# Performance work log

Measured on AMD Instinct MI355X. Metric: run time of the kernel, lower is better.

The kernel has to match this reference:

```python
import jax, jax.numpy as jnp
import numpy as np

DT = 0.02          # full control timestep (cfg dt)
N_SUBSTEPS = 8     # RK4 substeps per forward call
LMBDA = 0.5        # first-order actuator lag gain
G_VEC = jnp.array([0.0, 0.0, -9.81], dtype=jnp.float32)
N_ENVS = 2097152


def setup_inputs() -> dict:
    key = jax.random.key(0)
    k1, k2 = jax.random.split(key)
    X0 = jax.random.normal(k1, (N_ENVS, 9), dtype=jnp.float32)
    U = jax.random.normal(k2, (N_ENVS, 3), dtype=jnp.float32)
    return {"X0": X0, "U": U}


def reference(X0, U):
    h = DT / N_SUBSTEPS  # substep size

    def dynamics(X):
        v = X[:, 3:6]
        a = X[:, 6:9]
        a_dot = LMBDA * (U - a) / DT   # actuator lag uses full dt, as in torch code
        # X_dot = [p_dot, v_dot, a_dot] = [v, a - g_vec, a_dot]
        return jnp.concatenate([v, a - G_VEC, a_dot], axis=-1)

    def rk4_step(X, _):
        k1 = dynamics(X)
        k2 = dynamics(X + 0.5 * h * k1)
        k3 = dynamics(X + 0.5 * h * k2)
        k4 = dynamics(X + h * k3)
        X_next = X + (h / 6.0) * (k1 + 2.0 * k2 + 2.0 * k3 + k4)
        return X_next, None

    X_final, _ = jax.lax.scan(rk4_step, X0, None, length=N_SUBSTEPS)
    return X_final
```

## Files before the change

kernel.cpp:

```cpp
#include <hip/hip_runtime.h>


#define THREADS 256
#define TILE 256
#define CHUNK 4

struct Coeffs {
    float P00, P01, P02;
    float P10, P11, P12;
    float P20, P21, P22;
    float Ku0, Ku1, Ku2;
    float Kg0, Kg1, Kg2;
};

__device__ __forceinline__ void barrier_lgkm() {
    asm volatile("s_waitcnt lgkmcnt(0)" ::: "memory");
    __builtin_amdgcn_s_barrier();
    asm volatile("" ::: "memory");
}

__device__ __forceinline__ void compute_env(const float* __restrict__ sx,
                                            const float* __restrict__ su,
                                            const Coeffs& cf, float r[9]) {
    #pragma unroll
    for (int k = 0; k < 3; ++k) {
        const float p = sx[k];
        const float v = sx[3 + k];
        const float a = sx[6 + k];
        const float u = su[k];
        const float g = (k == 2) ? -9.81f : 0.0f;
        r[k]     = cf.P00 * p + cf.P01 * v + cf.P02 * a + cf.Ku0 * u + cf.Kg0 * g;
        r[3 + k] = cf.P10 * p + cf.P11 * v + cf.P12 * a + cf.Ku1 * u + cf.Kg1 * g;
        r[6 + k] = cf.P20 * p + cf.P21 * v + cf.P22 * a + cf.Ku2 * u + cf.Kg2 * g;
    }
}

__global__ __launch_bounds__(THREADS)
void pointmass_kernel(const float* __restrict__ X0,
                      const float* __restrict__ U,
                      float* __restrict__ Out,
                      int envTotal, Coeffs cf) {
    __shared__ float s_x[2][TILE * 9];
    __shared__ float s_u[2][TILE * 3];

    const int t = threadIdx.x;
    const int tileTotal = (envTotal + TILE - 1) / TILE;
    const int tb = blockIdx.x * CHUNK;
    if (tb >= tileTotal) return;
    const int te = min(tb + CHUNK, tileTotal);

    const bool allFull = (te * TILE <= envTotal);

    if (allFull) {
        const float4* X4 = (const float4*)X0;
        const float4* U4 = (const float4*)U;
        float4* O4 = (float4*)Out;

        {
            const size_t xb = (size_t)tb * 576;
            const size_t ub = (size_t)tb * 192;
            float4 a0 = X4[xb + t];
            float4 a1 = X4[xb + t + 256];
            float4 a2 = make_float4(0.f, 0.f, 0.f, 0.f);
            float4 b0 = make_float4(0.f, 0.f, 0.f, 0.f);
            if (t < 64)  a2 = X4[xb + t + 512];
            if (t < 192) b0 = U4[ub + t];
            ((float4*)s_x[0])[t]       = a0;
            ((float4*)s_x[0])[t + 256] = a1;
            if (t < 64)  ((float4*)s_x[0])[t + 512] = a2;
            if (t < 192) ((float4*)s_u[0])[t]       = b0;
        }
        barrier_lgkm();

        int cur = 0;
        for (int i = tb; i < te; ++i) {
            const bool haveNext = (i + 1 < te);

            float4 a0, a1;
            float4 a2 = make_float4(0.f, 0.f, 0.f, 0.f);
            float4 b0 = make_float4(0.f, 0.f, 0.f, 0.f);
            if (haveNext) {
                const size_t xb = (size_t)(i + 1) * 576;
                const size_t ub = (size_t)(i + 1) * 192;
                a0 = X4[xb + t];
                a1 = X4[xb + t + 256];
                if (t < 64)  a2 = X4[xb + t + 512];
                if (t < 192) b0 = U4[ub + t];
            }

            {
                float r[9];
                compute_env(s_x[cur] + t * 9, s_u[cur] + t * 3, cf, r);
                float* sxw = s_x[cur] + t * 9;
                #pragma unroll
                for (int q = 0; q < 9; ++q) sxw[q] = r[q];
            }
            barrier_lgkm();

            {
                const size_t ob = (size_t)i * 576;
                O4[ob + t]       = ((const float4*)s_x[cur])[t];
                O4[ob + t + 256] = ((const float4*)s_x[cur])[t + 256];
                if (t < 64) O4[ob + t + 512] = ((const float4*)s_x[cur])[t + 512];
            }

            if (haveNext) {
                const int nxt = cur ^ 1;
                ((float4*)s_x[nxt])[t]       = a0;
                ((float4*)s_x[nxt])[t + 256] = a1;
                if (t < 64)  ((float4*)s_x[nxt])[t + 512] = a2;
                if (t < 192) ((float4*)s_u[nxt])[t]       = b0;
                barrier_lgkm();
                cur = nxt;
            }
        }
    } else {
        for (int i = tb; i < te; ++i) {
            const int base = i * TILE;
            const int n = min(TILE, envTotal - base);
            __syncthreads();
            for (int j = t; j < n * 9; j += THREADS)
                s_x[0][j] = X0[(size_t)base * 9 + j];
            for (int j = t; j < n * 3; j += THREADS)
                s_u[0][j] = U[(size_t)base * 3 + j];
            __syncthreads();
            if (t < n) {
                float r[9];
                compute_env(s_x[0] + t * 9, s_u[0] + t * 3, cf, r);
                #pragma unroll
                for (int q = 0; q < 9; ++q)
                    Out[((size_t)base + t) * 9 + q] = r[q];
            }
        }
    }
}

static void mat3_mul(const double A[3][3], const double B[3][3], double C[3][3]) {
    for (int i = 0; i < 3; ++i)
        for (int j = 0; j < 3; ++j) {
            double s = 0.0;
            for (int k = 0; k < 3; ++k) s += A[i][k] * B[k][j];
            C[i][j] = s;
        }
}
static void mat3_copy(const double A[3][3], double B[3][3]) {
    for (int i = 0; i < 3; ++i) for (int j = 0; j < 3; ++j) B[i][j] = A[i][j];
}

extern "C" void kernel_launch(void* const* d_in, const int* in_sizes, int n_in,
                              void* d_out, int out_size, void* d_ws, size_t ws_size,
                              hipStream_t stream) {
    const float* X0 = (const float*)d_in[0];
    const float* U  = (const float*)d_in[1];
    float* Out = (float*)d_out;
    const int envTotal = in_sizes[0] / 9;

    const double DT = 0.02;
    const double h = DT / 8.0;
    const double c = 0.5 / DT;
    double hA[3][3] = {{0, h, 0}, {0, 0, h}, {0, 0, -c * h}};

    double hA2[3][3], hA3[3][3], hA4[3][3];
    mat3_mul(hA, hA, hA2);
    mat3_mul(hA2, hA, hA3);
    mat3_mul(hA3, hA, hA4);

    double P[3][3], Q[3][3];
    for (int i = 0; i < 3; ++i)
        for (int j = 0; j < 3; ++j) {
            const double I = (i == j) ? 1.0 : 0.0;
            P[i][j] = I + hA[i][j] + hA2[i][j] / 2.0 + hA3[i][j] / 6.0 + hA4[i][j] / 24.0;
            Q[i][j] = h * (I + hA[i][j] / 2.0 + hA2[i][j] / 6.0 + hA3[i][j] / 24.0);
        }

    double P2[3][3], P4[3][3], P8[3][3];
    mat3_mul(P, P, P2);
    mat3_mul(P2, P2, P4);
    mat3_mul(P4, P4, P8);

    double IP[3][3], IP2[3][3], IP4[3][3], T[3][3], S[3][3], R[3][3];
    mat3_copy(P, IP);  mat3_copy(P2, IP2);  mat3_copy(P4, IP4);
    for (int i = 0; i < 3; ++i) { IP[i][i] += 1.0; IP2[i][i] += 1.0; IP4[i][i] += 1.0; }
    mat3_mul(IP, IP2, T);
    mat3_mul(T, IP4, S);
    mat3_mul(S, Q, R);

    Coeffs cf;
    cf.P00 = (float)P8[0][0]; cf.P01 = (float)P8[0][1]; cf.P02 = (float)P8[0][2];
    cf.P10 = (float)P8[1][0]; cf.P11 = (float)P8[1][1]; cf.P12 = (float)P8[1][2];
    cf.P20 = (float)P8[2][0]; cf.P21 = (float)P8[2][1]; cf.P22 = (float)P8[2][2];
    cf.Ku0 = (float)(R[0][2] * c); cf.Ku1 = (float)(R[1][2] * c); cf.Ku2 = (float)(R[2][2] * c);
    cf.Kg0 = (float)(-R[0][1]);    cf.Kg1 = (float)(-R[1][1]);    cf.Kg2 = (float)(-R[2][1]);

    const int tileTotal = (envTotal + TILE - 1) / TILE;
    const int blocks = (tileTotal + CHUNK - 1) / CHUNK;
    pointmass_kernel<<<blocks, THREADS, 0, stream>>>(X0, U, Out, envTotal, cf);
}
```

Measured before the change: 157.0 us.

## Make each wavefront own private LDS tiles to drop block-wide barriers

Each 64-lane wavefront now stages and processes its own 64-environment tiles in a private LDS slice, so the block-wide s_barrier calls are removed. Waves then progress independently, and the same double-buffered prefetch is kept per wave. A sched_barrier keeps the compiler from reordering the next-tile LDS writes ahead of the output reads. Trade-offs: the global load and store granularity per wave gets smaller, and the tail is handled by a simple scalar path in the last block.

Result: no change. 156.1 us (-0.5%).

```diff
diff --git a/kernel.cpp b/kernel.cpp
--- a/kernel.cpp
+++ b/kernel.cpp
@@ -2,8 +2,11 @@
 
 
 #define THREADS 256
-#define TILE 256
+#define WAVES 4
+#define WTILE 64
 #define CHUNK 4
+#define XF4 144
+#define UF4 48
 
 struct Coeffs {
     float P00, P01, P02;
@@ -12,12 +15,6 @@
     float Ku0, Ku1, Ku2;
     float Kg0, Kg1, Kg2;
 };
-
-__device__ __forceinline__ void barrier_lgkm() {
-    asm volatile("s_waitcnt lgkmcnt(0)" ::: "memory");
-    __builtin_amdgcn_s_barrier();
-    asm volatile("" ::: "memory");
-}
 
 __device__ __forceinline__ void compute_env(const float* __restrict__ sx,
                                             const float* __restrict__ su,
@@ -40,97 +37,98 @@
                       const float* __restrict__ U,
                       float* __restrict__ Out,
                       int envTotal, Coeffs cf) {
-    __shared__ float s_x[2][TILE * 9];
-    __shared__ float s_u[2][TILE * 3];
+    __shared__ float lds[2][WAVES][768];
 
     const int t = threadIdx.x;
-    const int tileTotal = (envTotal + TILE - 1) / TILE;
-    const int tb = blockIdx.x * CHUNK;
-    if (tb >= tileTotal) return;
-    const int te = min(tb + CHUNK, tileTotal);
+    const int w = t >> 6;
+    const int l = t & 63;
+    const int fullTiles = envTotal / WTILE;
+    const int tileBase = (blockIdx.x * WAVES + w) * CHUNK;
+    const int te = min(tileBase + CHUNK, fullTiles);
 
-    const bool allFull = (te * TILE <= envTotal);
+    const float4* X4 = (const float4*)X0;
+    const float4* U4 = (const float4*)U;
+    float4* O4 = (float4*)Out;
 
-    if (allFull) {
-        const float4* X4 = (const float4*)X0;
-        const float4* U4 = (const float4*)U;
-        float4* O4 = (float4*)Out;
+    if (tileBase < te) {
+        float* const xs0 = &lds[0][w][0];
+        float* const us0 = &lds[0][w][576];
+        float* const xs1 = &lds[1][w][0];
+        float* const us1 = &lds[1][w][576];
 
         {
-            const size_t xb = (size_t)tb * 576;
-            const size_t ub = (size_t)tb * 192;
-            float4 a0 = X4[xb + t];
-            float4 a1 = X4[xb + t + 256];
+            const size_t xb = (size_t)tileBase * XF4;
+            const size_t ub = (size_t)tileBase * UF4;
+            float4 a0 = X4[xb + l];
+            float4 a1 = X4[xb + 64 + l];
             float4 a2 = make_float4(0.f, 0.f, 0.f, 0.f);
             float4 b0 = make_float4(0.f, 0.f, 0.f, 0.f);
-            if (t < 64)  a2 = X4[xb + t + 512];
-            if (t < 192) b0 = U4[ub + t];
-            ((float4*)s_x[0])[t]       = a0;
-            ((float4*)s_x[0])[t + 256] = a1;
-            if (t < 64)  ((float4*)s_x[0])[t + 512] = a2;
-            if (t < 192) ((float4*)s_u[0])[t]       = b0;
+            if (l < 16) a2 = X4[xb + 128 + l];
+            if (l < 48) b0 = U4[ub + l];
+            ((float4*)xs0)[l]      = a0;
+            ((float4*)xs0)[64 + l] = a1;
+            if (l < 16) ((float4*)xs0)[128 + l] = a2;
+            if (l < 48) ((float4*)us0)[l]       = b0;
         }
-        barrier_lgkm();
 
         int cur = 0;
-        for (int i = tb; i < te; ++i) {
+        for (int i = tileBase; i < te; ++i) {
+            float* const xs  = cur ? xs1 : xs0;
+            float* const us  = cur ? us1 : us0;
+            float* const xsN = cur ? xs0 : xs1;
+            float* const usN = cur ? us0 : us1;
             const bool haveNext = (i + 1 < te);
 
             float4 a0, a1;
             float4 a2 = make_float4(0.f, 0.f, 0.f, 0.f);
             float4 b0 = make_float4(0.f, 0.f, 0.f, 0.f);
             if (haveNext) {
-                const size_t xb = (size_t)(i + 1) * 576;
-                const size_t ub = (size_t)(i + 1) * 192;
-                a0 = X4[xb + t];
-                a1 = X4[xb + t + 256];
-                if (t < 64)  a2 = X4[xb + t + 512];
-                if (t < 192) b0 = U4[ub + t];
+                const size_t xb = (size_t)(i + 1) * XF4;
+                const size_t ub = (size_t)(i + 1) * UF4;
+                a0 = X4[xb + l];
+                a1 = X4[xb + 64 + l];
+                if (l < 16) a2 = X4[xb + 128 + l];
+                if (l < 48) b0 = U4[ub + l];
             }
 
             {
                 float r[9];
-                compute_env(s_x[cur] + t * 9, s_u[cur] + t * 3, cf, r);
-                float* sxw = s_x[cur] + t * 9;
+                compute_env(xs + l * 9, us + l * 3, cf, r);
+                float* sxw = xs + l * 9;
                 #pragma unroll
                 for (int q = 0; q < 9; ++q) sxw[q] = r[q];
             }
-            barrier_lgkm();
 
             {
-                const size_t ob = (size_t)i * 576;
-                O4[ob + t]       = ((const float4*)s_x[cur])[t];
-                O4[ob + t + 256] = ((const float4*)s_x[cur])[t + 256];
-                if (t < 64) O4[ob + t + 512] = ((const float4*)s_x[cur])[t + 512];
+                const size_t ob = (size_t)i * XF4;
+                O4[ob + l]      = ((const float4*)xs)[l];
+                O4[ob + 64 + l] = ((const float4*)xs)[64 + l];
+                if (l < 16) O4[ob + 128 + l] = ((const float4*)xs)[128 + l];
             }
 
+            __builtin_amdgcn_sched_barrier(0);
+
             if (haveNext) {
-                const int nxt = cur ^ 1;
-                ((float4*)s_x[nxt])[t]       = a0;
-                ((float4*)s_x[nxt])[t + 256] = a1;
-                if (t < 64)  ((float4*)s_x[nxt])[t + 512] = a2;
-                if (t < 192) ((float4*)s_u[nxt])[t]       = b0;
-                barrier_lgkm();
-                cur = nxt;
+                ((float4*)xsN)[l]      = a0;
+                ((float4*)xsN)[64 + l] = a1;
+                if (l < 16) ((float4*)xsN)[128 + l] = a2;
+                if (l < 48) ((float4*)usN)[l]       = b0;
             }
+            cur ^= 1;
         }
-    } else {
-        for (int i = tb; i < te; ++i) {
-            const int base = i * TILE;
-            const int n = min(TILE, envTotal - base);
-            __syncthreads();
-            for (int j = t; j < n * 9; j += THREADS)
-                s_x[0][j] = X0[(size_t)base * 9 + j];
-            for (int j = t; j < n * 3; j += THREADS)
-                s_u[0][j] = U[(size_t)base * 3 + j];
-            __syncthreads();
-            if (t < n) {
-                float r[9];
-                compute_env(s_x[0] + t * 9, s_u[0] + t * 3, cf, r);
-                #pragma unroll
-                for (int q = 0; q < 9; ++q)
-                    Out[((size_t)base + t) * 9 + q] = r[q];
-            }
+    }
+
+    const int rem0 = fullTiles * WTILE;
+    if (rem0 < envTotal && blockIdx.x == gridDim.x - 1) {
+        for (int e = rem0 + t; e < envTotal; e += THREADS) {
+            float xr[9], ur[3], r[9];
+            #pragma unroll
+            for (int q = 0; q < 9; ++q) xr[q] = X0[(size_t)e * 9 + q];
+            #pragma unroll
+            for (int k = 0; k < 3; ++k) ur[k] = U[(size_t)e * 3 + k];
+            compute_env(xr, ur, cf, r);
+            #pragma unroll
+            for (int q = 0; q < 9; ++q) Out[(size_t)e * 9 + q] = r[q];
         }
     }
 }
@@ -192,7 +190,9 @@
     cf.Ku0 = (float)(R[0][2] * c); cf.Ku1 = (float)(R[1][2] * c); cf.Ku2 = (float)(R[2][2] * c);
     cf.Kg0 = (float)(-R[0][1]);    cf.Kg1 = (float)(-R[1][1]);    cf.Kg2 = (float)(-R[2][1]);
 
-    const int tileTotal = (envTotal + TILE - 1) / TILE;
-    const int blocks = (tileTotal + CHUNK - 1) / CHUNK;
+    const int fullTiles = envTotal / WTILE;
+    const int wavesNeeded = (fullTiles + CHUNK - 1) / CHUNK;
+    int blocks = (wavesNeeded + WAVES - 1) / WAVES;
+    if (blocks < 1) blocks = 1;
     pointmass_kernel<<<blocks, THREADS, 0, stream>>>(X0, U, Out, envTotal, cf);
 }
```
